# Kernel optimization log

Measured on AMD Instinct MI355X. Metric: run time of the kernel, lower is better.

Reference implementation:

```python
import jax, jax.numpy as jnp
import numpy as np


def setup_inputs() -> dict:
    key = jax.random.key(0)
    k1, k2 = jax.random.split(key)
    N, D = 65536, 512
    feeds = jax.random.normal(k1, (N, D), dtype=jnp.float32)
    feeds_repeat_times = jax.random.randint(k2, (N,), 0, 8)
    return {
        "feeds": feeds,
        "feeds_repeat_times": feeds_repeat_times,
        "output_feeds_size": 262144,
    }


def reference(feeds, feeds_repeat_times, output_feeds_size):
    # Equivalent of the per-row repeat + cat + pad + truncate, as one fused gather.
    # Output row j comes from source row i where cumsum(repeats) first exceeds j.
    cum = jnp.cumsum(feeds_repeat_times)          # [N]
    total = cum[-1]                               # total repeated rows
    pos = jnp.arange(output_feeds_size)           # [S]
    idx = jnp.searchsorted(cum, pos, side="right")  # source row per output row
    valid = pos < total                           # rows beyond total are zero pad
    idx = jnp.clip(idx, 0, feeds.shape[0] - 1)
    out = jnp.where(valid[:, None], feeds[idx], jnp.zeros((), dtype=feeds.dtype))
    return out
```

## Files before the change

kernel.cpp:

```cpp
#include <hip/hip_runtime.h>

#define NROWS 65536
#define DCOLS 512
#define D4    128

__global__ __launch_bounds__(1024) void scan_kernel(const int* __restrict__ rep,
                                                    int* __restrict__ cum) {
    __shared__ int sdata[1024];
    const int t = threadIdx.x;
    const int base = t * 64;

    int v[64];
    const int4* rep4 = (const int4*)(rep + base);
#pragma unroll
    for (int k = 0; k < 16; ++k) {
        int4 x = rep4[k];
        v[4 * k + 0] = x.x; v[4 * k + 1] = x.y;
        v[4 * k + 2] = x.z; v[4 * k + 3] = x.w;
    }
    int partial = 0;
#pragma unroll
    for (int k = 0; k < 64; ++k) partial += v[k];

    sdata[t] = partial;
    __syncthreads();
    for (int off = 1; off < 1024; off <<= 1) {
        int add = (t >= off) ? sdata[t - off] : 0;
        __syncthreads();
        sdata[t] += add;
        __syncthreads();
    }
    int running = sdata[t] - partial;
#pragma unroll
    for (int k = 0; k < 64; ++k) { running += v[k]; v[k] = running; }

    int4* cum4 = (int4*)(cum + base);
#pragma unroll
    for (int k = 0; k < 16; ++k) {
        int4 x;
        x.x = v[4 * k + 0]; x.y = v[4 * k + 1];
        x.z = v[4 * k + 2]; x.w = v[4 * k + 3];
        cum4[k] = x;
    }
}

__global__ __launch_bounds__(256) void zero_tail_kernel(const int* __restrict__ cum,
                                                        float4* __restrict__ out,
                                                        int S) {
    int total = cum[NROWS - 1];
    if (total > S) total = S;
    const long long startE = (long long)total * D4;
    const long long endE   = (long long)S * D4;
    const long long stride = (long long)gridDim.x * blockDim.x;
    const float4 z = make_float4(0.f, 0.f, 0.f, 0.f);
    for (long long e = startE + (long long)blockIdx.x * blockDim.x + threadIdx.x;
         e < endE; e += stride) {
        out[e] = z;
    }
}

__global__ __launch_bounds__(256) void scatter_kernel(const float* __restrict__ feeds,
                                                      const int* __restrict__ rep,
                                                      const int* __restrict__ cum,
                                                      float* __restrict__ out,
                                                      int S) {
    const int wave = (int)((blockIdx.x * blockDim.x + threadIdx.x) >> 6);
    const int lane = threadIdx.x & 63;
    if (wave >= NROWS) return;

    const int r = rep[wave];
    if (r == 0) return;
    const int end   = cum[wave];
    const int start = end - r;
    if (start >= S) return;

    const float4* src = (const float4*)(feeds + (long long)wave * DCOLS);
    const float4 a = src[lane];
    const float4 b = src[lane + 64];

    const int stop = end < S ? end : S;
    for (int j = start; j < stop; ++j) {
        float4* dst = (float4*)(out + (long long)j * DCOLS);
        dst[lane]      = a;
        dst[lane + 64] = b;
    }
}

extern "C" void kernel_launch(void* const* d_in, const int* in_sizes, int n_in,
                              void* d_out, int out_size, void* d_ws, size_t ws_size,
                              hipStream_t stream) {
    const float* feeds = (const float*)d_in[0];
    const int*   rep   = (const int*)d_in[1];
    const int S = out_size / DCOLS;

    int* cum = (int*)d_ws;

    scan_kernel<<<1, 1024, 0, stream>>>(rep, cum);
    zero_tail_kernel<<<2048, 256, 0, stream>>>(cum, (float4*)d_out, S);
    scatter_kernel<<<NROWS / 4, 256, 0, stream>>>(feeds, rep, cum, (float*)d_out, S);
}
```

Baseline: 628.0 us.

## Replace row scatter with index build plus per-output-row gather using nontemporal stores

Replaces the source-row scatter and the separate zero-tail kernel with two new kernels. The first writes the source row index for each output row. The second gathers one output row per wave and writes zeros for rows past the total, so each output row is written exactly once with coalesced nontemporal stores. The aim is to avoid load imbalance from rows repeated up to seven times and the extra zeroing pass, at the cost of an index build pass and re-reading repeated source rows.

```diff
diff --git a/kernel.cpp b/kernel.cpp
--- a/kernel.cpp
+++ b/kernel.cpp
@@ -3,6 +3,8 @@
 #define NROWS 65536
 #define DCOLS 512
 #define D4    128
+
+typedef float f32x4 __attribute__((ext_vector_type(4)));
 
 __global__ __launch_bounds__(1024) void scan_kernel(const int* __restrict__ rep,
                                                     int* __restrict__ cum) {
@@ -10,17 +12,14 @@
     const int t = threadIdx.x;
     const int base = t * 64;
 
-    int v[64];
+    int4 v[16];
     const int4* rep4 = (const int4*)(rep + base);
 #pragma unroll
-    for (int k = 0; k < 16; ++k) {
-        int4 x = rep4[k];
-        v[4 * k + 0] = x.x; v[4 * k + 1] = x.y;
-        v[4 * k + 2] = x.z; v[4 * k + 3] = x.w;
-    }
+    for (int k = 0; k < 16; ++k) v[k] = rep4[k];
+
     int partial = 0;
 #pragma unroll
-    for (int k = 0; k < 64; ++k) partial += v[k];
+    for (int k = 0; k < 16; ++k) partial += v[k].x + v[k].y + v[k].z + v[k].w;
 
     sdata[t] = partial;
     __syncthreads();
@@ -31,59 +30,55 @@
         __syncthreads();
     }
     int running = sdata[t] - partial;
-#pragma unroll
-    for (int k = 0; k < 64; ++k) { running += v[k]; v[k] = running; }
 
     int4* cum4 = (int4*)(cum + base);
 #pragma unroll
     for (int k = 0; k < 16; ++k) {
         int4 x;
-        x.x = v[4 * k + 0]; x.y = v[4 * k + 1];
-        x.z = v[4 * k + 2]; x.w = v[4 * k + 3];
+        running += v[k].x; x.x = running;
+        running += v[k].y; x.y = running;
+        running += v[k].z; x.z = running;
+        running += v[k].w; x.w = running;
         cum4[k] = x;
     }
 }
 
-__global__ __launch_bounds__(256) void zero_tail_kernel(const int* __restrict__ cum,
-                                                        float4* __restrict__ out,
+__global__ __launch_bounds__(256) void build_idx_kernel(const int* __restrict__ rep,
+                                                        const int* __restrict__ cum,
+                                                        int* __restrict__ idx,
                                                         int S) {
-    int total = cum[NROWS - 1];
-    if (total > S) total = S;
-    const long long startE = (long long)total * D4;
-    const long long endE   = (long long)S * D4;
-    const long long stride = (long long)gridDim.x * blockDim.x;
-    const float4 z = make_float4(0.f, 0.f, 0.f, 0.f);
-    for (long long e = startE + (long long)blockIdx.x * blockDim.x + threadIdx.x;
-         e < endE; e += stride) {
-        out[e] = z;
-    }
+    const int i = blockIdx.x * blockDim.x + threadIdx.x;
+    if (i >= NROWS) return;
+    const int end   = cum[i];
+    const int r     = rep[i];
+    const int start = end - r;
+    if (r == 0 || start >= S) return;
+    const int stop = end < S ? end : S;
+    for (int j = start; j < stop; ++j) idx[j] = i;
 }
 
-__global__ __launch_bounds__(256) void scatter_kernel(const float* __restrict__ feeds,
-                                                      const int* __restrict__ rep,
-                                                      const int* __restrict__ cum,
-                                                      float* __restrict__ out,
-                                                      int S) {
+__global__ __launch_bounds__(256) void gather_kernel(const f32x4* __restrict__ feeds,
+                                                     const int* __restrict__ idx,
+                                                     const int* __restrict__ cum,
+                                                     f32x4* __restrict__ out,
+                                                     int S) {
     const int wave = (int)((blockIdx.x * blockDim.x + threadIdx.x) >> 6);
     const int lane = threadIdx.x & 63;
-    if (wave >= NROWS) return;
+    if (wave >= S) return;
 
-    const int r = rep[wave];
-    if (r == 0) return;
-    const int end   = cum[wave];
-    const int start = end - r;
-    if (start >= S) return;
+    const int total = cum[NROWS - 1];
 
-    const float4* src = (const float4*)(feeds + (long long)wave * DCOLS);
-    const float4 a = src[lane];
-    const float4 b = src[lane + 64];
-
-    const int stop = end < S ? end : S;
-    for (int j = start; j < stop; ++j) {
-        float4* dst = (float4*)(out + (long long)j * DCOLS);
-        dst[lane]      = a;
-        dst[lane + 64] = b;
+    f32x4 a = (f32x4)0.f;
+    f32x4 b = (f32x4)0.f;
+    if (wave < total) {
+        const int si = idx[wave];
+        const f32x4* src = feeds + (long long)si * D4;
+        a = src[lane];
+        b = src[lane + 64];
     }
+    f32x4* dst = out + (long long)wave * D4;
+    __builtin_nontemporal_store(a, dst + lane);
+    __builtin_nontemporal_store(b, dst + lane + 64);
 }
 
 extern "C" void kernel_launch(void* const* d_in, const int* in_sizes, int n_in,
@@ -94,8 +89,10 @@
     const int S = out_size / DCOLS;
 
     int* cum = (int*)d_ws;
+    int* idx = (int*)d_ws + NROWS;
 
     scan_kernel<<<1, 1024, 0, stream>>>(rep, cum);
-    zero_tail_kernel<<<2048, 256, 0, stream>>>(cum, (float4*)d_out, S);
-    scatter_kernel<<<NROWS / 4, 256, 0, stream>>>(feeds, rep, cum, (float*)d_out, S);
+    build_idx_kernel<<<NROWS / 256, 256, 0, stream>>>(rep, cum, idx, S);
+    gather_kernel<<<S / 4, 256, 0, stream>>>((const f32x4*)feeds, idx, cum,
+                                             (f32x4*)d_out, S);
 }
```

Result: faster. 608.7 us (-3.1%).
